# Optimization experiments

Measured on AMD Instinct MI355X. Metric: run time of the kernel, lower is better.

Reference implementation:

```python
import jax, jax.numpy as jnp
import numpy as np
import math

B, S, E = 16, 4096, 16      # batch, seq_len, n_experts
NE = 64                     # config.n_embd -> expert bottleneck dim
F = 4 * NE                  # n_state = 4*n_embd -> token feature dim


def gelu(x):
    # tanh-approx GELU exactly as in the source module
    c = math.sqrt(2.0 / math.pi)
    return 0.5 * x * (1.0 + jnp.tanh(c * (x + 0.044715 * x * x * x)))


def setup_inputs() -> dict:
    key = jax.random.key(0)
    ks = jax.random.split(key, 7)
    s1 = 1.0 / math.sqrt(F)   # fan-in init like nn.Linear(F, NE)
    s2 = 1.0 / math.sqrt(NE)  # fan-in init like nn.Linear(NE, F)
    return {
        "x":  jax.random.normal(ks[0], (B, S, F), jnp.float32),
        "W1": jax.random.uniform(ks[1], (E, F, NE), jnp.float32, -s1, s1),  # stacked c_fc
        "b1": jax.random.uniform(ks[2], (E, NE),    jnp.float32, -s1, s1),
        "W2": jax.random.uniform(ks[3], (E, NE, F), jnp.float32, -s2, s2),  # stacked c_proj
        "b2": jax.random.uniform(ks[4], (E, F),     jnp.float32, -s2, s2),
        "Wg": jax.random.uniform(ks[5], (F, E),     jnp.float32, -s1, s1),  # router
        "bg": jax.random.uniform(ks[6], (E,),       jnp.float32, -s1, s1),
    }


def reference(x, W1, b1, W2, b2, Wg, bg):
    # Router: per-token scores -> mean over sequence -> softmax over experts. [B, E]
    gate = jax.nn.softmax(jnp.mean(x @ Wg + bg, axis=1), axis=-1)
    # Dense all-experts FFN: [B, E, S, NE]
    h = gelu(jnp.einsum('bsf,efh->besh', x, W1) + b1[None, :, None, :])
    # [B, E, S, F]
    outs = jnp.einsum('besh,ehf->besf', h, W2) + b2[None, :, None, :]
    # Gate-weighted combine over experts -> [B, S, F]
    return jnp.einsum('be,besf->bsf', gate, outs)
```

## Files before the change

### kernel.cpp

```cpp
#include <hip/hip_runtime.h>
#include <hip/hip_bf16.h>
#include <stdint.h>

#define NB 16
#define NS 4096
#define NF 256
#define NH 64
#define NEXP 16

typedef __attribute__((ext_vector_type(8))) short     bf16x8;
typedef __attribute__((ext_vector_type(4))) float     f32x4;
typedef __attribute__((ext_vector_type(2))) unsigned  u32x2;
typedef __attribute__((ext_vector_type(8))) unsigned short u16x8;

#define PART_OFF   0u
#define GATE_OFF   524288u
#define BIASC_OFF  525312u
#define W1T_OFF    541696u
#define W2T_OFF    1065984u

__device__ __forceinline__ unsigned short bfr(float f) {
  unsigned u = __float_as_uint(f);
  u += 0x7fffu + ((u >> 16) & 1u);
  return (unsigned short)(u >> 16);
}
__device__ __forceinline__ unsigned pk(float a, float b) {
  __hip_bfloat162 t = __float22bfloat162_rn(make_float2(a, b));
  union { __hip_bfloat162 h; unsigned u; } cv; cv.h = t; return cv.u;
}
__device__ __forceinline__ void stage16(const void* g, void* l) {
  __builtin_amdgcn_global_load_lds((const __attribute__((address_space(1))) void*)g,
                                   (__attribute__((address_space(3))) void*)l, 16, 0, 0);
}

__global__ void k_pre(const float* __restrict__ x, const float* __restrict__ W1,
                      const float* __restrict__ W2, uint8_t* __restrict__ wsb) {
  const int blk = blockIdx.x;
  if (blk < 512) {
    const int b  = blk >> 5;
    const int ch = blk & 31;
    const int f  = threadIdx.x;
    const float* xp = x + ((size_t)b * NS + (size_t)ch * 128) * NF + f;
    float s = 0.0f;
    for (int i = 0; i < 128; ++i) s += xp[(size_t)i * NF];
    ((float*)(wsb + PART_OFF))[(size_t)(ch * 16 + b) * NF + f] = s;
    return;
  }
  const int u = (blk - 512) * 256 + threadIdx.x;
  u16x8 vals;
  if (u < 32768) {
    const int e  = u >> 11;
    const int r  = u & 2047;
    const int hd = r >> 5;
    const int kc = r & 31;
    const float* src = W1 + (size_t)e * (NF * NH) + (size_t)(kc * 8) * NH + hd;
#pragma unroll
    for (int j = 0; j < 8; ++j) vals[j] = bfr(src[(size_t)j * NH]);
    const int dst = (kc >> 2) * 4096 + hd * 64 + (kc & 3) * 16;
    *(u16x8*)(wsb + W1T_OFF + (size_t)e * 32768 + dst) = vals;
  } else {
    const int u2 = u - 32768;
    const int e  = u2 >> 11;
    const int r  = u2 & 2047;
    const int f  = r >> 3;
    const int hc = r & 7;
    const float* src = W2 + (size_t)e * (NH * NF) + (size_t)(hc * 8) * NF + f;
#pragma unroll
    for (int j = 0; j < 8; ++j) vals[j] = bfr(src[(size_t)j * NF]);
    const int dst = hc * 4096 + f * 16;
    *(u16x8*)(wsb + W2T_OFF + (size_t)e * 32768 + dst) = vals;
  }
}

__global__ void k_gate(const float* __restrict__ Wg, const float* __restrict__ bg,
                       const float* __restrict__ b2, uint8_t* __restrict__ wsb) {
  __shared__ float cs[16][256];
  __shared__ float lg[16][16];
  __shared__ float gs[16][16];
  const float* part  = (const float*)(wsb + PART_OFF);
  float* gate  = (float*)(wsb + GATE_OFF);
  float* biasc = (float*)(wsb + BIASC_OFF);
  const int t = threadIdx.x;
  for (int b = 0; b < 16; ++b) {
    float s = 0.0f;
    for (int ch = 0; ch < 32; ++ch) s += part[(size_t)(ch * 16 + b) * NF + t];
    cs[b][t] = s * (1.0f / 4096.0f);
  }
  __syncthreads();
  {
    const int b = t >> 4, e = t & 15;
    float acc = bg[e];
    for (int f = 0; f < NF; ++f) acc += cs[b][f] * Wg[f * 16 + e];
    lg[b][e] = acc;
  }
  __syncthreads();
  {
    const int b = t >> 4, e = t & 15;
    float m = lg[b][0];
    for (int j = 1; j < 16; ++j) m = fmaxf(m, lg[b][j]);
    float den = 0.0f;
    for (int j = 0; j < 16; ++j) den += __expf(lg[b][j] - m);
    float g = __expf(lg[b][e] - m) / den;
    gate[b * 16 + e] = g;
    gs[b][e] = g;
  }
  __syncthreads();
  for (int b = 0; b < 16; ++b) {
    float acc = 0.0f;
    for (int e = 0; e < 16; ++e) acc += gs[b][e] * b2[e * NF + t];
    biasc[b * NF + t] = acc;
  }
}

__global__ __launch_bounds__(512, 2)
void k_main(const float* __restrict__ x, const float* __restrict__ b1g,
            const uint8_t* __restrict__ wsb, float* __restrict__ out) {
  __shared__ __align__(16) uint8_t lds[163840];

  const int tid  = threadIdx.x;
  const int w    = tid >> 6;
  const int lane = tid & 63;
  const int c    = lane & 15;
  const int q    = lane >> 4;
  const int wh   = w & 1;
  const int wt   = w >> 1;
  const int wf2  = w >> 1;
  const int wt2  = w & 1;
  const int blk  = blockIdx.x;
  const int b    = blk >> 5;

  const float* gate_ws = (const float*)(wsb + GATE_OFF) + b * 16;
  const float* biasc   = (const float*)(wsb + BIASC_OFF) + b * NF;
  const uint8_t* w1src = wsb + W1T_OFF;
  const uint8_t* w2src = wsb + W2T_OFF;

#pragma unroll
  for (int i = 0; i < 4; ++i)
    stage16(w1src + i * 8192 + tid * 16, lds + i * 8192 + tid * 16);

  bf16x8 xf[2][8];
  {
    const int row0 = blk * 128 + wt * 32;
#pragma unroll
    for (int n = 0; n < 2; ++n) {
      const float* xp = x + (size_t)(row0 + n * 16 + c) * NF + q * 8;
#pragma unroll
      for (int ks = 0; ks < 8; ++ks) {
        f32x4 v0 = *(const f32x4*)(xp + ks * 32);
        f32x4 v1 = *(const f32x4*)(xp + ks * 32 + 4);
        union { unsigned u[4]; bf16x8 v; } cv;
        cv.u[0] = pk(v0[0], v0[1]); cv.u[1] = pk(v0[2], v0[3]);
        cv.u[2] = pk(v1[0], v1[1]); cv.u[3] = pk(v1[2], v1[3]);
        xf[n][ks] = cv.v;
      }
    }
  }

  const f32x4 fzero = {0.0f, 0.0f, 0.0f, 0.0f};
  f32x4 acc2[4][4];
#pragma unroll
  for (int i = 0; i < 4; ++i)
#pragma unroll
    for (int j = 0; j < 4; ++j) acc2[i][j] = fzero;

  __syncthreads();

  const float K1 = -2.3021858962f;
  const float KA = -0.102942243f;

#pragma unroll 1
  for (int e = 0; e < NEXP; ++e) {
    const int p  = e & 1;
    const int pn = p ^ 1;

    if (e < 15) {
      const uint8_t* src = w1src + (size_t)(e + 1) * 32768;
      uint8_t* dst = lds + pn * 32768;
#pragma unroll
      for (int i = 0; i < 4; ++i)
        stage16(src + i * 8192 + tid * 16, dst + i * 8192 + tid * 16);
    }
    {
      const uint8_t* src = w2src + (size_t)e * 32768;
      uint8_t* dst = lds + 65536 + p * 32768;
#pragma unroll
      for (int i = 0; i < 4; ++i)
        stage16(src + i * 8192 + tid * 16, dst + i * 8192 + tid * 16);
    }

    const uint8_t* w1p = lds + p * 32768;
    f32x4 acc1[2][2];
    acc1[0][0] = fzero; acc1[0][1] = fzero; acc1[1][0] = fzero; acc1[1][1] = fzero;
#pragma unroll
    for (int ks = 0; ks < 8; ++ks) {
      bf16x8 a0 = *(const bf16x8*)(w1p + ks * 4096 + (wh * 32 + c) * 64 + q * 16);
      bf16x8 a1 = *(const bf16x8*)(w1p + ks * 4096 + (wh * 32 + 16 + c) * 64 + q * 16);
      acc1[0][0] = __builtin_amdgcn_mfma_f32_16x16x32_bf16(a0, xf[0][ks], acc1[0][0], 0, 0, 0);
      acc1[0][1] = __builtin_amdgcn_mfma_f32_16x16x32_bf16(a0, xf[1][ks], acc1[0][1], 0, 0, 0);
      acc1[1][0] = __builtin_amdgcn_mfma_f32_16x16x32_bf16(a1, xf[0][ks], acc1[1][0], 0, 0, 0);
      acc1[1][1] = __builtin_amdgcn_mfma_f32_16x16x32_bf16(a1, xf[1][ks], acc1[1][1], 0, 0, 0);
    }

    if (e > 0) {
      const uint8_t* w2p  = lds + 65536 + pn * 32768;
      const uint8_t* htp2 = lds + 131072 + pn * 16384;
#pragma unroll
      for (int ks2 = 0; ks2 < 2; ++ks2) {
        bf16x8 bb2[4];
#pragma unroll
        for (int n2 = 0; n2 < 4; ++n2)
          bb2[n2] = *(const bf16x8*)(htp2 + (ks2 * 4 + q) * 2048 + (wt2 * 64 + n2 * 16 + c) * 16);
#pragma unroll
        for (int m2 = 0; m2 < 4; ++m2) {
          bf16x8 a2 = *(const bf16x8*)(w2p + (ks2 * 4 + q) * 4096 + (wf2 * 64 + m2 * 16 + c) * 16);
#pragma unroll
          for (int n2 = 0; n2 < 4; ++n2)
            acc2[m2][n2] = __builtin_amdgcn_mfma_f32_16x16x32_bf16(a2, bb2[n2], acc2[m2][n2], 0, 0, 0);
        }
      }
    }

    {
      const float gv = gate_ws[e];
      uint8_t* htp = lds + 131072 + p * 16384;
      f32x4 b1v[2];
#pragma unroll
      for (int m = 0; m < 2; ++m)
        b1v[m] = *(const f32x4*)(b1g + e * NH + wh * 32 + m * 16 + q * 4);
#pragma unroll
      for (int m = 0; m < 2; ++m) {
#pragma unroll
        for (int n = 0; n < 2; ++n) {
          f32x4 hv = acc1[m][n] + b1v[m];
          float o[4];
#pragma unroll
          for (int r = 0; r < 4; ++r) {
            float xx = hv[r];
            float x2 = xx * xx;
            float tt = fmaf(KA, x2, K1);
            float ez = __builtin_amdgcn_exp2f(xx * tt);
            float rc = __builtin_amdgcn_rcpf(ez + 1.0f);
            o[r] = (gv * xx) * rc;
          }
          u32x2 hw;
          hw.x = pk(o[0], o[1]);
          hw.y = pk(o[2], o[3]);
          const int chunk = wh * 4 + m * 2 + (q >> 1);
          const int tok   = wt * 32 + n * 16 + c;
          *(u32x2*)(htp + chunk * 2048 + tok * 16 + (q & 1) * 8) = hw;
        }
      }
    }

    __syncthreads();
  }

  {
    const uint8_t* w2p  = lds + 65536 + 32768;
    const uint8_t* htp2 = lds + 131072 + 16384;
#pragma unroll
    for (int ks2 = 0; ks2 < 2; ++ks2) {
      bf16x8 bb2[4];
#pragma unroll
      for (int n2 = 0; n2 < 4; ++n2)
        bb2[n2] = *(const bf16x8*)(htp2 + (ks2 * 4 + q) * 2048 + (wt2 * 64 + n2 * 16 + c) * 16);
#pragma unroll
      for (int m2 = 0; m2 < 4; ++m2) {
        bf16x8 a2 = *(const bf16x8*)(w2p + (ks2 * 4 + q) * 4096 + (wf2 * 64 + m2 * 16 + c) * 16);
#pragma unroll
        for (int n2 = 0; n2 < 4; ++n2)
          acc2[m2][n2] = __builtin_amdgcn_mfma_f32_16x16x32_bf16(a2, bb2[n2], acc2[m2][n2], 0, 0, 0);
      }
    }
  }

#pragma unroll
  for (int m2 = 0; m2 < 4; ++m2) {
    const int fbase = wf2 * 64 + m2 * 16 + q * 4;
    f32x4 bc = *(const f32x4*)(biasc + fbase);
#pragma unroll
    for (int n2 = 0; n2 < 4; ++n2) {
      const int token = blk * 128 + wt2 * 64 + n2 * 16 + c;
      f32x4 o = acc2[m2][n2] + bc;
      *(f32x4*)(out + (size_t)token * NF + fbase) = o;
    }
  }
}

extern "C" void kernel_launch(void* const* d_in, const int* in_sizes, int n_in,
                              void* d_out, int out_size, void* d_ws, size_t ws_size,
                              hipStream_t stream) {
  const float* x  = (const float*)d_in[0];
  const float* W1 = (const float*)d_in[1];
  const float* b1 = (const float*)d_in[2];
  const float* W2 = (const float*)d_in[3];
  const float* b2 = (const float*)d_in[4];
  const float* Wg = (const float*)d_in[5];
  const float* bg = (const float*)d_in[6];
  float* out = (float*)d_out;
  uint8_t* wsb = (uint8_t*)d_ws;

  k_pre<<<768, 256, 0, stream>>>(x, W1, W2, wsb);
  k_gate<<<1, 256, 0, stream>>>(Wg, bg, b2, wsb);
  k_main<<<512, 512, 0, stream>>>(x, b1, wsb, out);
}
```

Before: 127.3 us.

## Load W2 fragments directly into registers instead of staging through LDS

W2 for each expert is now read from global memory straight into per-wave registers, one iteration ahead, instead of being copied into a double-buffered LDS region. This shrinks LDS from 160KB to 96KB and removes the LDS write/read traffic for W2. The full __syncthreads is replaced by a partial vmcnt wait plus s_barrier so the W2 register loads can stay in flight across the barrier. The change also adds scheduling barriers and setprio around the MFMA block. In exchange, each wave now issues its own global loads for W2 (duplicated across waves sharing wf2) and holds more registers, which may pressure occupancy at 512 threads with 2 blocks per CU.

Measured after the change: 136.2 us. 1.07x slower.

```diff
diff --git a/kernel.cpp b/kernel.cpp
--- a/kernel.cpp
+++ b/kernel.cpp
@@ -115,7 +115,7 @@
 __global__ __launch_bounds__(512, 2)
 void k_main(const float* __restrict__ x, const float* __restrict__ b1g,
             const uint8_t* __restrict__ wsb, float* __restrict__ out) {
-  __shared__ __align__(16) uint8_t lds[163840];
+  __shared__ __align__(16) uint8_t lds[98304];
 
   const int tid  = threadIdx.x;
   const int w    = tid >> 6;
@@ -134,6 +134,8 @@
   const uint8_t* w1src = wsb + W1T_OFF;
   const uint8_t* w2src = wsb + W2T_OFF;
 
+  const int w2fo = q * 4096 + (wf2 * 64 + c) * 16;
+
 #pragma unroll
   for (int i = 0; i < 4; ++i)
     stage16(w1src + i * 8192 + tid * 16, lds + i * 8192 + tid * 16);
@@ -163,6 +165,8 @@
 #pragma unroll
     for (int j = 0; j < 4; ++j) acc2[i][j] = fzero;
 
+  bf16x8 w2r[2][4];
+
   __syncthreads();
 
   const float K1 = -2.3021858962f;
@@ -180,17 +184,22 @@
       for (int i = 0; i < 4; ++i)
         stage16(src + i * 8192 + tid * 16, dst + i * 8192 + tid * 16);
     }
-    {
-      const uint8_t* src = w2src + (size_t)e * 32768;
-      uint8_t* dst = lds + 65536 + p * 32768;
-#pragma unroll
-      for (int i = 0; i < 4; ++i)
-        stage16(src + i * 8192 + tid * 16, dst + i * 8192 + tid * 16);
+    __builtin_amdgcn_sched_barrier(0x38F);
+
+    bf16x8 bb2[2][4];
+    if (e > 0) {
+      const uint8_t* htp2 = lds + 65536 + pn * 16384;
+#pragma unroll
+      for (int ks2 = 0; ks2 < 2; ++ks2)
+#pragma unroll
+        for (int n2 = 0; n2 < 4; ++n2)
+          bb2[ks2][n2] = *(const bf16x8*)(htp2 + (ks2 * 4 + q) * 2048 + (wt2 * 64 + n2 * 16 + c) * 16);
     }
 
     const uint8_t* w1p = lds + p * 32768;
     f32x4 acc1[2][2];
     acc1[0][0] = fzero; acc1[0][1] = fzero; acc1[1][0] = fzero; acc1[1][1] = fzero;
+    __builtin_amdgcn_s_setprio(1);
 #pragma unroll
     for (int ks = 0; ks < 8; ++ks) {
       bf16x8 a0 = *(const bf16x8*)(w1p + ks * 4096 + (wh * 32 + c) * 64 + q * 16);
@@ -200,29 +209,29 @@
       acc1[1][0] = __builtin_amdgcn_mfma_f32_16x16x32_bf16(a1, xf[0][ks], acc1[1][0], 0, 0, 0);
       acc1[1][1] = __builtin_amdgcn_mfma_f32_16x16x32_bf16(a1, xf[1][ks], acc1[1][1], 0, 0, 0);
     }
-
     if (e > 0) {
-      const uint8_t* w2p  = lds + 65536 + pn * 32768;
-      const uint8_t* htp2 = lds + 131072 + pn * 16384;
-#pragma unroll
-      for (int ks2 = 0; ks2 < 2; ++ks2) {
-        bf16x8 bb2[4];
-#pragma unroll
-        for (int n2 = 0; n2 < 4; ++n2)
-          bb2[n2] = *(const bf16x8*)(htp2 + (ks2 * 4 + q) * 2048 + (wt2 * 64 + n2 * 16 + c) * 16);
-#pragma unroll
-        for (int m2 = 0; m2 < 4; ++m2) {
-          bf16x8 a2 = *(const bf16x8*)(w2p + (ks2 * 4 + q) * 4096 + (wf2 * 64 + m2 * 16 + c) * 16);
+#pragma unroll
+      for (int ks2 = 0; ks2 < 2; ++ks2)
+#pragma unroll
+        for (int m2 = 0; m2 < 4; ++m2)
 #pragma unroll
           for (int n2 = 0; n2 < 4; ++n2)
-            acc2[m2][n2] = __builtin_amdgcn_mfma_f32_16x16x32_bf16(a2, bb2[n2], acc2[m2][n2], 0, 0, 0);
-        }
-      }
+            acc2[m2][n2] = __builtin_amdgcn_mfma_f32_16x16x32_bf16(w2r[ks2][m2], bb2[ks2][n2], acc2[m2][n2], 0, 0, 0);
+    }
+    __builtin_amdgcn_s_setprio(0);
+
+    {
+      const uint8_t* src = w2src + (size_t)e * 32768 + w2fo;
+#pragma unroll
+      for (int ks2 = 0; ks2 < 2; ++ks2)
+#pragma unroll
+        for (int m2 = 0; m2 < 4; ++m2)
+          w2r[ks2][m2] = *(const bf16x8*)(src + ks2 * 16384 + m2 * 256);
     }
 
     {
       const float gv = gate_ws[e];
-      uint8_t* htp = lds + 131072 + p * 16384;
+      uint8_t* htp = lds + 65536 + p * 16384;
       f32x4 b1v[2];
 #pragma unroll
       for (int m = 0; m < 2; ++m)
@@ -252,12 +261,13 @@
       }
     }
 
-    __syncthreads();
+    asm volatile("s_waitcnt vmcnt(8) lgkmcnt(0)" ::: "memory");
+    __builtin_amdgcn_s_barrier();
+    __builtin_amdgcn_sched_barrier(0);
   }
 
   {
-    const uint8_t* w2p  = lds + 65536 + 32768;
-    const uint8_t* htp2 = lds + 131072 + 16384;
+    const uint8_t* htp2 = lds + 65536 + 16384;
 #pragma unroll
     for (int ks2 = 0; ks2 < 2; ++ks2) {
       bf16x8 bb2[4];
@@ -265,12 +275,10 @@
       for (int n2 = 0; n2 < 4; ++n2)
         bb2[n2] = *(const bf16x8*)(htp2 + (ks2 * 4 + q) * 2048 + (wt2 * 64 + n2 * 16 + c) * 16);
 #pragma unroll
-      for (int m2 = 0; m2 < 4; ++m2) {
-        bf16x8 a2 = *(const bf16x8*)(w2p + (ks2 * 4 + q) * 4096 + (wf2 * 64 + m2 * 16 + c) * 16);
+      for (int m2 = 0; m2 < 4; ++m2)
 #pragma unroll
         for (int n2 = 0; n2 < 4; ++n2)
-          acc2[m2][n2] = __builtin_amdgcn_mfma_f32_16x16x32_bf16(a2, bb2[n2], acc2[m2][n2], 0, 0, 0);
-      }
+          acc2[m2][n2] = __builtin_amdgcn_mfma_f32_16x16x32_bf16(w2r[ks2][m2], bb2[n2], acc2[m2][n2], 0, 0, 0);
     }
   }
 
```
